# Performance work log

Measured on AMD Instinct MI355X. Metric: run time of the kernel, lower is better.

Reference implementation:

```python
import jax, jax.numpy as jnp
import numpy as np

B, T_NEW, CACHED_MAX = 8, 128, 2048
D_MODEL, N_HEADS = 1024, 16
D_HEAD = D_MODEL // N_HEADS
MAX_TOTAL = CACHED_MAX + T_NEW


def rotate_half(x):
    x1, x2 = x[..., : x.shape[-1] // 2], x[..., x.shape[-1] // 2 :]
    return jnp.concatenate([-x2, x1], axis=-1)


def setup_inputs() -> dict:
    key = jax.random.key(0)
    ks = jax.random.split(key, 16)
    w_scale = D_MODEL ** -0.5  # xavier-ish
    inp = {
        "x_new": jax.random.normal(ks[0], (B, T_NEW, D_MODEL), jnp.float32),
        "past_k": jax.random.normal(ks[1], (B, N_HEADS, CACHED_MAX, D_HEAD), jnp.float32),
        "past_v": jax.random.normal(ks[2], (B, N_HEADS, CACHED_MAX, D_HEAD), jnp.float32),
        "Wq": jax.random.normal(ks[3], (D_MODEL, D_MODEL), jnp.float32) * w_scale,
        "bq": jnp.zeros((D_MODEL,), jnp.float32),
        "Wk": jax.random.normal(ks[4], (D_MODEL, D_MODEL), jnp.float32) * w_scale,
        "bk": jnp.zeros((D_MODEL,), jnp.float32),
        "Wv": jax.random.normal(ks[5], (D_MODEL, D_MODEL), jnp.float32) * w_scale,
        "bv": jnp.zeros((D_MODEL,), jnp.float32),
        "Wo": jax.random.normal(ks[6], (D_MODEL, D_MODEL), jnp.float32) * w_scale,
        "bo": jnp.zeros((D_MODEL,), jnp.float32),
        "inv_freq": 1.0 / (10000.0 ** (jnp.arange(0, D_HEAD, 2, dtype=jnp.float32) / D_HEAD)),
        # ragged lengths; >=1 so every row attends to something
        "past_lengths": jax.random.randint(ks[7], (B,), 1, CACHED_MAX + 1),
        "new_lengths": jax.random.randint(ks[8], (B,), 1, T_NEW + 1),
    }
    return inp


def _attention_fwd(x_new, past_k, past_v, Wq, bq, Wk, bk, Wv, bv, Wo, bo, inv_freq,
                   past_lengths, new_lengths):
    steps = jnp.arange(T_NEW)
    valid_new = steps[None, :] < new_lengths[:, None]            # [B, T_new]

    def proj(W, b):  # torch Linear: x @ W.T + b -> [B, H, T_new, D_head]
        y = jnp.einsum("btm,nm->btn", x_new, W) + b
        return y.reshape(B, T_NEW, N_HEADS, D_HEAD).transpose(0, 2, 1, 3)

    q, k_new, v_new = proj(Wq, bq), proj(Wk, bk), proj(Wv, bv)

    # RoPE at absolute positions past_len + step (0 where invalid)
    positions = jnp.where(valid_new, past_lengths[:, None] + steps[None, :], 0)
    freqs = positions[..., None].astype(jnp.float32) * inv_freq  # [B, T_new, D_head/2]
    emb = jnp.concatenate([freqs, freqs], axis=-1)               # [B, T_new, D_head]
    cos = jnp.cos(emb)[:, None]                                  # [B, 1, T_new, D_head]
    sin = jnp.sin(emb)[:, None]
    q = q * cos + rotate_half(q) * sin
    k_new = k_new * cos + rotate_half(k_new) * sin

    vm = valid_new[:, None, :, None].astype(q.dtype)
    q, k_new, v_new = q * vm, k_new * vm, v_new * vm

    total_lengths = past_lengths + new_lengths
    j = jnp.arange(MAX_TOTAL)
    in_past = (j[None, :] < past_lengths[:, None])[:, None, :, None]       # [B,1,MT,1]
    in_new = ((j[None, :] >= past_lengths[:, None]) &
              (j[None, :] < total_lengths[:, None]))[:, None, :, None]
    idx_new = jnp.clip(j[None, :] - past_lengths[:, None], 0, T_NEW - 1)   # [B, MT]

    past_k_pad = jnp.pad(past_k, ((0, 0), (0, 0), (0, T_NEW), (0, 0)))
    past_v_pad = jnp.pad(past_v, ((0, 0), (0, 0), (0, T_NEW), (0, 0)))
    gather = jax.vmap(lambda xb, ib: xb[:, ib])  # [H,T_new,D], [MT] -> [H,MT,D]
    k_total = jnp.where(in_past, past_k_pad, jnp.where(in_new, gather(k_new, idx_new), 0.0))
    v_total = jnp.where(in_past, past_v_pad, jnp.where(in_new, gather(v_new, idx_new), 0.0))

    attend = j[None, :] < total_lengths[:, None]                  # [B, MT]
    scores = jnp.einsum("bhqd,bhkd->bhqk", q, k_total) * (D_HEAD ** -0.5)
    neg = jnp.asarray(jnp.finfo(scores.dtype).min, scores.dtype)
    scores = jnp.where(attend[:, None, None, :], scores, neg)
    attn = jax.nn.softmax(scores, axis=-1)
    ctx = jnp.einsum("bhqk,bhkd->bhqd", attn, v_total)            # [B,H,T_new,D]

    out = ctx.transpose(0, 2, 1, 3).reshape(B, T_NEW, D_MODEL)
    out = jnp.einsum("btm,nm->btn", out, Wo) + bo
    return out * valid_new[..., None].astype(out.dtype)


def reference(x_new, past_k, past_v, Wq, bq, Wk, bk, Wv, bv, Wo, bo, inv_freq,
              past_lengths, new_lengths):
    return _attention_fwd(x_new, past_k, past_v, Wq, bq, Wk, bk, Wv, bv, Wo, bo,
                          inv_freq, past_lengths, new_lengths)
```

## Files before the change

### kernel.cpp

```cpp
#include <hip/hip_runtime.h>

#define NB 8
#define TNEW 128
#define CMAX 2048
#define DMODEL 1024
#define NH 16
#define DH 64

typedef float f32x4 __attribute__((ext_vector_type(4)));
typedef short short8 __attribute__((ext_vector_type(8)));
typedef short short4v __attribute__((ext_vector_type(4)));

__device__ __forceinline__ short f2bf(float x) {
  unsigned u = __float_as_uint(x);
  u += 0x7FFFu + ((u >> 16) & 1u);
  return (short)(u >> 16);
}
__device__ __forceinline__ float bf2f(short s) {
  return __uint_as_float(((unsigned)(unsigned short)s) << 16);
}
__device__ __forceinline__ short8 cvt8(f32x4 a, f32x4 b) {
  short8 o;
  o[0] = f2bf(a.x); o[1] = f2bf(a.y); o[2] = f2bf(a.z); o[3] = f2bf(a.w);
  o[4] = f2bf(b.x); o[5] = f2bf(b.y); o[6] = f2bf(b.z); o[7] = f2bf(b.w);
  return o;
}

#define LGKM0_BAR()                                            \
  __builtin_amdgcn_sched_barrier(0);                           \
  asm volatile("s_waitcnt lgkmcnt(0)" ::: "memory");           \
  __builtin_amdgcn_sched_barrier(0);                           \
  __builtin_amdgcn_s_barrier()
#define TAIL_BAR()                                             \
  __builtin_amdgcn_sched_barrier(0);                           \
  __builtin_amdgcn_s_barrier()

__global__ __launch_bounds__(256) void cvt5_bf16(
    const float* __restrict__ s0, const float* __restrict__ s1,
    const float* __restrict__ s2, const float* __restrict__ s3,
    const float* __restrict__ s4, short* __restrict__ dst) {
  const int seg = blockIdx.x >> 10;
  const int i = (blockIdx.x & 1023) * 256 + threadIdx.x;
  const float* src = seg == 0 ? s0 : seg == 1 ? s1 : seg == 2 ? s2 : seg == 3 ? s3 : s4;
  f32x4 v = *(const f32x4*)(src + (size_t)i * 4);
  short4v o;
  o.x = f2bf(v.x); o.y = f2bf(v.y); o.z = f2bf(v.z); o.w = f2bf(v.w);
  *(short4v*)(dst + (size_t)seg * (1u << 20) + (size_t)i * 4) = o;
}

template<int MODE>
__global__ __launch_bounds__(256) void gemm64(
    const short* __restrict__ A, const short* __restrict__ Wbase,
    void* __restrict__ Out, const float* __restrict__ bias0,
    const float* __restrict__ bias1, const float* __restrict__ bias2,
    const int* __restrict__ new_len)
{
  constexpr int LDT = 40;
  __shared__ short As[64 * LDT];
  __shared__ short Bs[64 * LDT];
  const int n0 = blockIdx.x * 64, m0 = blockIdx.y * 64, z = blockIdx.z;
  if (MODE == 0 && (m0 & 64) && new_len[m0 >> 7] <= 64) return;
  const short* Wp = Wbase + (size_t)z * (DMODEL * DMODEL);
  const float* bias = (MODE == 0) ? (z == 0 ? bias0 : (z == 1 ? bias1 : bias2)) : bias0;
  const int tid = threadIdx.x, lane = tid & 63, w = tid >> 6;
  const int wm = (w >> 1) * 32, wn = (w & 1) * 32;
  const int lr = lane & 15, lk = lane >> 4;

  const int srow = tid >> 2, soff = (tid & 3) * 8;
  const short* Ag = A  + (size_t)(m0 + srow) * DMODEL + soff;
  const short* Bg = Wp + (size_t)(n0 + srow) * DMODEL + soff;
  short* Al = As + srow * LDT + soff;
  short* Bl = Bs + srow * LDT + soff;

  short8 va0 = *(const short8*)(Ag);
  short8 vb0 = *(const short8*)(Bg);
  short8 va1, vb1;
  f32x4 acc[2][2] = {};

#define GEMM_PHASE(CURA, CURB, NXTA, NXTB, KNEXT)                          \
  {                                                                        \
    *(short8*)Al = CURA;                                                   \
    *(short8*)Bl = CURB;                                                   \
    NXTA = *(const short8*)(Ag + (KNEXT) * 32);                            \
    NXTB = *(const short8*)(Bg + (KNEXT) * 32);                            \
    LGKM0_BAR();                                                           \
    short8 af0 = *(const short8*)(As + (wm + lr) * LDT + lk * 8);          \
    short8 af1 = *(const short8*)(As + (wm + 16 + lr) * LDT + lk * 8);     \
    short8 bg0 = *(const short8*)(Bs + (wn + lr) * LDT + lk * 8);          \
    short8 bg1 = *(const short8*)(Bs + (wn + 16 + lr) * LDT + lk * 8);     \
    acc[0][0] = __builtin_amdgcn_mfma_f32_16x16x32_bf16(af0, bg0, acc[0][0], 0, 0, 0); \
    acc[0][1] = __builtin_amdgcn_mfma_f32_16x16x32_bf16(af0, bg1, acc[0][1], 0, 0, 0); \
    acc[1][0] = __builtin_amdgcn_mfma_f32_16x16x32_bf16(af1, bg0, acc[1][0], 0, 0, 0); \
    acc[1][1] = __builtin_amdgcn_mfma_f32_16x16x32_bf16(af1, bg1, acc[1][1], 0, 0, 0); \
    TAIL_BAR();                                                            \
  }

  for (int kt = 0; kt < DMODEL / 32; kt += 2) {
    const int k1 = kt + 1;
    const int k2 = (kt + 2 < DMODEL / 32) ? kt + 2 : DMODEL / 32 - 1;
    GEMM_PHASE(va0, vb0, va1, vb1, k1);
    GEMM_PHASE(va1, vb1, va0, vb0, k2);
  }
#undef GEMM_PHASE

#pragma unroll
  for (int i = 0; i < 2; ++i) {
#pragma unroll
    for (int j = 0; j < 2; ++j) {
      const int col = n0 + wn + j * 16 + lr;
      const float bcol = bias[col];
#pragma unroll
      for (int r = 0; r < 4; ++r) {
        const int row = m0 + wm + i * 16 + lk * 4 + r;
        float v = acc[i][j][r] + bcol;
        if (MODE == 0) {
          ((short*)Out)[(size_t)z * (NB * TNEW * DMODEL) + (size_t)row * DMODEL + col] = f2bf(v);
        } else {
          const int bb = row >> 7, t = row & 127;
          ((float*)Out)[(size_t)row * DMODEL + col] = (t < new_len[bb]) ? v : 0.0f;
        }
      }
    }
  }
}

__global__ __launch_bounds__(256) void rope_mask(
    short* __restrict__ qb, short* __restrict__ kb, short* __restrict__ vb,
    const float* __restrict__ inv_freq, const int* __restrict__ past_len,
    const int* __restrict__ new_len)
{
  const int idx = blockIdx.x * 256 + threadIdx.x;
  const int d = idx & 31;
  const int h = (idx >> 5) & 15;
  const int t = (idx >> 9) & 127;
  const int b = idx >> 16;
  const bool valid = t < new_len[b];
  const float pos = (float)(past_len[b] + t);
  float sn, cs;
  sincosf(pos * inv_freq[d], &sn, &cs);
  const size_t base = (size_t)(b * 128 + t) * DMODEL + h * 64 + d;
  const float q1 = bf2f(qb[base]), q2 = bf2f(qb[base + 32]);
  const float k1 = bf2f(kb[base]), k2 = bf2f(kb[base + 32]);
  qb[base]      = valid ? f2bf(q1 * cs - q2 * sn) : (short)0;
  qb[base + 32] = valid ? f2bf(q2 * cs + q1 * sn) : (short)0;
  kb[base]      = valid ? f2bf(k1 * cs - k2 * sn) : (short)0;
  kb[base + 32] = valid ? f2bf(k2 * cs + k1 * sn) : (short)0;
  if (!valid) { vb[base] = 0; vb[base + 32] = 0; }
}

__global__ __launch_bounds__(512) void attn_split(
    const float* __restrict__ pk, const float* __restrict__ pv,
    const short* __restrict__ qb, const short* __restrict__ kb,
    const short* __restrict__ vb, float* __restrict__ Opart,
    float* __restrict__ Ml, const int* __restrict__ past_len,
    const int* __restrict__ new_len, int splits)
{
  constexpr int LDT = 72;
  __shared__ short Kl[64 * LDT];
  __shared__ short Vt[64 * LDT];
  __shared__ short Pl[128 * LDT];
  const int bh = blockIdx.x, b = bh >> 4, h = bh & 15;
  const int s = blockIdx.y;
  const int past = past_len[b];
  const int nlen = new_len[b];
  const int total = past + nlen;
  const int tid = threadIdx.x, lane = tid & 63, w = tid >> 6;
  const int lr = lane & 15, lk = lane >> 4;

  const int nt = (total + 63) >> 6;

  float* mlp = Ml + (size_t)(bh * splits + s) * 256;
  float* op  = Opart + (size_t)(bh * splits + s) * (128 * 64);

  if (s >= nt) {
#pragma unroll
    for (int r = 0; r < 4; ++r) {
      const int q = w * 16 + lk * 4 + r;
      if (lr == 0) { mlp[q] = -3.0e38f; mlp[128 + q] = 0.f; }
    }
    return;
  }

  const bool wvalid = (w * 16) < nlen;
  short8 qf0 = {}, qf1 = {};
  if (wvalid) {
    const short* qrow = qb + (size_t)(b * 128 + w * 16 + lr) * DMODEL + h * 64;
    qf0 = *(const short8*)(qrow + lk * 8);
    qf1 = *(const short8*)(qrow + 32 + lk * 8);
  }
  float m_run[4], l_run[4];
  f32x4 acc[4] = {};
#pragma unroll
  for (int r = 0; r < 4; ++r) { m_run[r] = -3.0e38f; l_run[r] = 0.f; }

  const int jr = tid >> 3, seg = tid & 7;
  const float* pkb = pk + ((size_t)(b * 16 + h) * CMAX) * 64 + seg * 8;
  const float* pvb = pv + ((size_t)(b * 16 + h) * CMAX) * 64 + seg * 8;
  const short* kbb = kb + (size_t)(b * 128) * DMODEL + h * 64 + seg * 8;
  const short* vbb = vb + (size_t)(b * 128) * DMODEL + h * 64 + seg * 8;

  f32x4 kA0 = {}, kB0 = {}, vA0 = {}, vB0 = {};
  f32x4 kA1 = {}, kB1 = {}, vA1 = {}, vB1 = {};
  int smode0 = 2, smode1 = 2;

#define STAGE_ISSUE(SET, T)                                                   \
  {                                                                           \
    const int j_ = (T) * 64 + jr;                                             \
    if (j_ < past) {                                                          \
      smode##SET = 0;                                                         \
      kA##SET = *(const f32x4*)(pkb + (size_t)j_ * 64);                       \
      kB##SET = *(const f32x4*)(pkb + (size_t)j_ * 64 + 4);                   \
      vA##SET = *(const f32x4*)(pvb + (size_t)j_ * 64);                       \
      vB##SET = *(const f32x4*)(pvb + (size_t)j_ * 64 + 4);                   \
    } else if (j_ < total) {                                                  \
      smode##SET = 1;                                                         \
      kA##SET = __builtin_bit_cast(f32x4, *(const short8*)(kbb + (size_t)(j_ - past) * DMODEL)); \
      vA##SET = __builtin_bit_cast(f32x4, *(const short8*)(vbb + (size_t)(j_ - past) * DMODEL)); \
    } else {                                                                  \
      smode##SET = 2;                                                         \
    }                                                                         \
  }

#define ATTN_TILE(SET, OTHER, KT)                                             \
  {                                                                           \
         \
    short8 kr = {}, vr = {};                                                  \
    if (smode##SET == 0) { kr = cvt8(kA##SET, kB##SET); vr = cvt8(vA##SET, vB##SET); } \
    else if (smode##SET == 1) { kr = __builtin_bit_cast(short8, kA##SET); vr = __builtin_bit_cast(short8, vA##SET); } \
    *(short8*)(Kl + jr * LDT + seg * 8) = kr;                                 \
    _Pragma("unroll")                                                         \
    for (int i = 0; i < 8; ++i) Vt[(seg * 8 + i) * LDT + (jr ^ (seg * 8))] = vr[i]; \
                    \
    STAGE_ISSUE(OTHER, (KT) + splits);                                        \
    LGKM0_BAR();                                                              \
    if (wvalid) {                                                             \
      f32x4 sc[4];                                                            \
      __builtin_amdgcn_s_setprio(1);                                          \
      _Pragma("unroll")                                                       \
      for (int nf = 0; nf < 4; ++nf) {                                        \
        short8 k0 = *(const short8*)(Kl + (nf * 16 + lr) * LDT + lk * 8);     \
        short8 k1 = *(const short8*)(Kl + (nf * 16 + lr) * LDT + 32 + lk * 8);\
        f32x4 zv = {};                                                        \
        zv = __builtin_amdgcn_mfma_f32_16x16x32_bf16(qf0, k0, zv, 0, 0, 0);   \
        sc[nf] = __builtin_amdgcn_mfma_f32_16x16x32_bf16(qf1, k1, zv, 0, 0, 0);\
      }                                                                       \
      __builtin_amdgcn_s_setprio(0);                                          \
      const int kg0 = (KT) * 64;                                              \
      float pmax[4] = {-3.0e38f, -3.0e38f, -3.0e38f, -3.0e38f};               \
      _Pragma("unroll")                                                       \
      for (int nf = 0; nf < 4; ++nf) {                                        \
        const bool ok = (kg0 + nf * 16 + lr) < total;                         \
        _Pragma("unroll")                                                     \
        for (int r = 0; r < 4; ++r) {                                         \
          const float sv = ok ? sc[nf][r] * 0.125f : -3.0e38f;                \
          sc[nf][r] = sv;                                                     \
          pmax[r] = fmaxf(pmax[r], sv);                                       \
        }                                                                     \
      }                                                                       \
      _Pragma("unroll")                                                       \
      for (int r = 0; r < 4; ++r) {                                           \
        _Pragma("unroll")                                                     \
        for (int off = 1; off < 16; off <<= 1)                                \
          pmax[r] = fmaxf(pmax[r], __shfl_xor(pmax[r], off));                 \
      }                                                                       \
      float alpha[4], rsum[4];                                                \
      _Pragma("unroll")                                                       \
      for (int r = 0; r < 4; ++r) {                                           \
        const float mn = fmaxf(m_run[r], pmax[r]);                            \
        alpha[r] = __expf(m_run[r] - mn);                                     \
        m_run[r] = mn;                                                        \
        rsum[r] = 0.f;                                                        \
      }                                                                       \
      _Pragma("unroll")                                                       \
      for (int nf = 0; nf < 4; ++nf)                                          \
        _Pragma("unroll")                                                     \
        for (int r = 0; r < 4; ++r) {                                         \
          const float p = __expf(sc[nf][r] - m_run[r]);                       \
          sc[nf][r] = p;                                                      \
          rsum[r] += p;                                                       \
        }                                                                     \
      _Pragma("unroll")                                                       \
      for (int r = 0; r < 4; ++r) {                                           \
        _Pragma("unroll")                                                     \
        for (int off = 1; off < 16; off <<= 1)                                \
          rsum[r] += __shfl_xor(rsum[r], off);                                \
        l_run[r] = l_run[r] * alpha[r] + rsum[r];                             \
      }                                                                       \
      _Pragma("unroll")                                                       \
      for (int nf = 0; nf < 4; ++nf)                                          \
        _Pragma("unroll")                                                     \
        for (int r = 0; r < 4; ++r) acc[nf][r] *= alpha[r];                   \
      _Pragma("unroll")                                                       \
      for (int nf = 0; nf < 4; ++nf)                                          \
        _Pragma("unroll")                                                     \
        for (int r = 0; r < 4; ++r)                                           \
          Pl[(w * 16 + lk * 4 + r) * LDT + nf * 16 + lr] = f2bf(sc[nf][r]);   \
      __builtin_amdgcn_s_setprio(1);                                          \
      _Pragma("unroll")                                                       \
      for (int kf = 0; kf < 2; ++kf) {                                        \
        short8 pf = *(const short8*)(Pl + (w * 16 + lr) * LDT + kf * 32 + lk * 8); \
        _Pragma("unroll")                                                     \
        for (int nf = 0; nf < 4; ++nf) {                                      \
          const int dd = nf * 16 + lr;                                        \
          short8 vf = *(const short8*)(Vt + dd * LDT + ((kf * 32 + lk * 8) ^ (dd & 56))); \
          acc[nf] = __builtin_amdgcn_mfma_f32_16x16x32_bf16(pf, vf, acc[nf], 0, 0, 0); \
        }                                                                     \
      }                                                                       \
      __builtin_amdgcn_s_setprio(0);                                          \
    }                                                                         \
    TAIL_BAR();                                                               \
  }

  STAGE_ISSUE(0, s);
  const int nIter = (nt - s + splits - 1) / splits;
  const int E = (nIter + 1) & ~1;
  for (int i = 0; i < E; i += 2) {
    const int kt0 = s + i * splits;
    ATTN_TILE(0, 1, kt0);
    ATTN_TILE(1, 0, kt0 + splits);
  }
#undef ATTN_TILE
#undef STAGE_ISSUE

  if (wvalid) {
#pragma unroll
    for (int nf = 0; nf < 4; ++nf)
#pragma unroll
      for (int r = 0; r < 4; ++r) {
        const int q = w * 16 + lk * 4 + r, d = nf * 16 + lr;
        op[(size_t)q * 64 + d] = acc[nf][r];
      }
#pragma unroll
    for (int r = 0; r < 4; ++r) {
      const int q = w * 16 + lk * 4 + r;
      if (lr == 0) { mlp[q] = m_run[r]; mlp[128 + q] = l_run[r]; }
    }
  } else {
#pragma unroll
    for (int r = 0; r < 4; ++r) {
      const int q = w * 16 + lk * 4 + r;
      if (lr == 0) { mlp[q] = -3.0e38f; mlp[128 + q] = 0.f; }
    }
  }
}

__global__ __launch_bounds__(256) void attn_combine(
    const float* __restrict__ Opart, const float* __restrict__ Ml,
    short* __restrict__ ctxb, const int* __restrict__ new_len, int splits)
{
  const int bh = blockIdx.x, b = bh >> 4, h = bh & 15;
  const int q = blockIdx.y * 16 + (threadIdx.x >> 4);
  if (q >= new_len[b]) return;
  const int dv = (threadIdx.x & 15) * 4;
  const float* mlb = Ml + (size_t)bh * splits * 256;
  float mstar = -3.0e38f;
  for (int s = 0; s < splits; ++s)
    mstar = fmaxf(mstar, mlb[s * 256 + q]);
  float lsum = 0.f;
  f32x4 o = {};
  for (int s = 0; s < splits; ++s) {
    const float ws = __expf(mlb[s * 256 + q] - mstar);
    lsum += ws * mlb[s * 256 + 128 + q];
    if (ws > 0.f) {
      f32x4 ov = *(const f32x4*)(Opart + ((size_t)(bh * splits + s) * 128 + q) * 64 + dv);
      o.x += ws * ov.x; o.y += ws * ov.y; o.z += ws * ov.z; o.w += ws * ov.w;
    }
  }
  const float inv = 1.0f / lsum;
  short4v r;
  r.x = f2bf(o.x * inv); r.y = f2bf(o.y * inv); r.z = f2bf(o.z * inv); r.w = f2bf(o.w * inv);
  *(short4v*)(ctxb + (size_t)(b * 128 + q) * DMODEL + h * 64 + dv) = r;
}

extern "C" void kernel_launch(void* const* d_in, const int* in_sizes, int n_in,
                              void* d_out, int out_size, void* d_ws, size_t ws_size,
                              hipStream_t stream) {
  const float* x      = (const float*)d_in[0];
  const float* past_k = (const float*)d_in[1];
  const float* past_v = (const float*)d_in[2];
  const float* Wq = (const float*)d_in[3];
  const float* bq = (const float*)d_in[4];
  const float* Wk = (const float*)d_in[5];
  const float* bk = (const float*)d_in[6];
  const float* Wv = (const float*)d_in[7];
  const float* bv = (const float*)d_in[8];
  const float* Wo = (const float*)d_in[9];
  const float* bo = (const float*)d_in[10];
  const float* inv_freq = (const float*)d_in[11];
  const int* past_len = (const int*)d_in[12];
  const int* new_len  = (const int*)d_in[13];

  short* wsb = (short*)d_ws;
  const size_t M1 = 1u << 20;
  short* Xb  = wsb;
  short* Wqb = wsb + 1 * M1;
  short* Wob = wsb + 4 * M1;
  short* qb  = wsb + 5 * M1;
  short* kb  = wsb + 6 * M1;
  short* vb  = wsb + 7 * M1;
  short* ctx = wsb + 8 * M1;
  float* Opart = (float*)(wsb + 9 * M1);

  int splits = 1;
  for (int s = 8; s >= 1; s >>= 1) {
    size_t need = 9 * M1 * sizeof(short) +
                  (size_t)s * 128 * (128 * 64 + 256) * sizeof(float);
    if (need <= ws_size) { splits = s; break; }
  }
  float* Ml = Opart + (size_t)128 * splits * (128 * 64);

  cvt5_bf16<<<5120, 256, 0, stream>>>(x, Wq, Wk, Wv, Wo, wsb);

  gemm64<0><<<dim3(16, 16, 3), 256, 0, stream>>>(Xb, Wqb, (void*)qb, bq, bk, bv, new_len);
  rope_mask<<<2048, 256, 0, stream>>>(qb, kb, vb, inv_freq, past_len, new_len);
  attn_split<<<dim3(128, splits), 512, 0, stream>>>(past_k, past_v, qb, kb, vb,
                                                    Opart, Ml, past_len, new_len, splits);
  attn_combine<<<dim3(128, 8), 256, 0, stream>>>(Opart, Ml, ctx, new_len, splits);
  gemm64<1><<<dim3(16, 16, 1), 256, 0, stream>>>(ctx, Wob, d_out, bo, nullptr, nullptr, new_len);
}
```

Baseline: 79.63 us.

## Fuse RoPE into QKV projection epilogue and flatten attention split grid

Removes the separate rope_mask kernel. The Q/K GEMM epilogue now applies the rotary embedding directly, using a changed warp column mapping so each lane holds both d and d+32 of a head. This removes one launch and a read-modify-write pass over the bf16 Q/K/V buffers. The attention launch is flattened to a 1D grid with splits interleaved per (batch, head), and a guard skips compute on tiles past the valid length. Invalid new-token rows of q/k/v are no longer explicitly zeroed, so the code now relies on downstream masking to keep them out of the result.

```diff
diff --git a/kernel.cpp b/kernel.cpp
--- a/kernel.cpp
+++ b/kernel.cpp
@@ -53,7 +53,8 @@
     const short* __restrict__ A, const short* __restrict__ Wbase,
     void* __restrict__ Out, const float* __restrict__ bias0,
     const float* __restrict__ bias1, const float* __restrict__ bias2,
-    const int* __restrict__ new_len)
+    const int* __restrict__ new_len, const float* __restrict__ inv_freq,
+    const int* __restrict__ past_len)
 {
   constexpr int LDT = 40;
   __shared__ short As[64 * LDT];
@@ -63,7 +64,7 @@
   const short* Wp = Wbase + (size_t)z * (DMODEL * DMODEL);
   const float* bias = (MODE == 0) ? (z == 0 ? bias0 : (z == 1 ? bias1 : bias2)) : bias0;
   const int tid = threadIdx.x, lane = tid & 63, w = tid >> 6;
-  const int wm = (w >> 1) * 32, wn = (w & 1) * 32;
+  const int wm = (w >> 1) * 32, wn2 = (w & 1) * 16;
   const int lr = lane & 15, lk = lane >> 4;
 
   const int srow = tid >> 2, soff = (tid & 3) * 8;
@@ -86,8 +87,8 @@
     LGKM0_BAR();                                                           \
     short8 af0 = *(const short8*)(As + (wm + lr) * LDT + lk * 8);          \
     short8 af1 = *(const short8*)(As + (wm + 16 + lr) * LDT + lk * 8);     \
-    short8 bg0 = *(const short8*)(Bs + (wn + lr) * LDT + lk * 8);          \
-    short8 bg1 = *(const short8*)(Bs + (wn + 16 + lr) * LDT + lk * 8);     \
+    short8 bg0 = *(const short8*)(Bs + (wn2 + lr) * LDT + lk * 8);         \
+    short8 bg1 = *(const short8*)(Bs + (wn2 + 32 + lr) * LDT + lk * 8);    \
     acc[0][0] = __builtin_amdgcn_mfma_f32_16x16x32_bf16(af0, bg0, acc[0][0], 0, 0, 0); \
     acc[0][1] = __builtin_amdgcn_mfma_f32_16x16x32_bf16(af0, bg1, acc[0][1], 0, 0, 0); \
     acc[1][0] = __builtin_amdgcn_mfma_f32_16x16x32_bf16(af1, bg0, acc[1][0], 0, 0, 0); \
@@ -103,49 +104,49 @@
   }
 #undef GEMM_PHASE
 
-#pragma unroll
-  for (int i = 0; i < 2; ++i) {
-#pragma unroll
-    for (int j = 0; j < 2; ++j) {
-      const int col = n0 + wn + j * 16 + lr;
-      const float bcol = bias[col];
+  const int colb = n0 + wn2 + lr;
+  const float b0 = bias[colb], b1 = bias[colb + 32];
+
+  if (MODE == 0 && z <= 1) {
+    const int bb = m0 >> 7;
+    const int pbase = past_len[bb];
+    const float fr = inv_freq[(wn2 + lr) & 31];
+    short* outp = (short*)Out + (size_t)z * (NB * TNEW * DMODEL);
+#pragma unroll
+    for (int i = 0; i < 2; ++i) {
 #pragma unroll
       for (int r = 0; r < 4; ++r) {
         const int row = m0 + wm + i * 16 + lk * 4 + r;
-        float v = acc[i][j][r] + bcol;
+        const float pos = (float)(pbase + (row & 127));
+        float sn, cs;
+        sincosf(pos * fr, &sn, &cs);
+        const float a0 = acc[i][0][r] + b0;
+        const float a1 = acc[i][1][r] + b1;
+        outp[(size_t)row * DMODEL + colb]      = f2bf(a0 * cs - a1 * sn);
+        outp[(size_t)row * DMODEL + colb + 32] = f2bf(a1 * cs + a0 * sn);
+      }
+    }
+  } else {
+#pragma unroll
+    for (int i = 0; i < 2; ++i) {
+#pragma unroll
+      for (int r = 0; r < 4; ++r) {
+        const int row = m0 + wm + i * 16 + lk * 4 + r;
+        const float a0 = acc[i][0][r] + b0;
+        const float a1 = acc[i][1][r] + b1;
         if (MODE == 0) {
-          ((short*)Out)[(size_t)z * (NB * TNEW * DMODEL) + (size_t)row * DMODEL + col] = f2bf(v);
+          short* outp = (short*)Out + (size_t)z * (NB * TNEW * DMODEL);
+          outp[(size_t)row * DMODEL + colb]      = f2bf(a0);
+          outp[(size_t)row * DMODEL + colb + 32] = f2bf(a1);
         } else {
           const int bb = row >> 7, t = row & 127;
-          ((float*)Out)[(size_t)row * DMODEL + col] = (t < new_len[bb]) ? v : 0.0f;
+          const bool ok = t < new_len[bb];
+          ((float*)Out)[(size_t)row * DMODEL + colb]      = ok ? a0 : 0.0f;
+          ((float*)Out)[(size_t)row * DMODEL + colb + 32] = ok ? a1 : 0.0f;
         }
       }
     }
   }
-}
-
-__global__ __launch_bounds__(256) void rope_mask(
-    short* __restrict__ qb, short* __restrict__ kb, short* __restrict__ vb,
-    const float* __restrict__ inv_freq, const int* __restrict__ past_len,
-    const int* __restrict__ new_len)
-{
-  const int idx = blockIdx.x * 256 + threadIdx.x;
-  const int d = idx & 31;
-  const int h = (idx >> 5) & 15;
-  const int t = (idx >> 9) & 127;
-  const int b = idx >> 16;
-  const bool valid = t < new_len[b];
-  const float pos = (float)(past_len[b] + t);
-  float sn, cs;
-  sincosf(pos * inv_freq[d], &sn, &cs);
-  const size_t base = (size_t)(b * 128 + t) * DMODEL + h * 64 + d;
-  const float q1 = bf2f(qb[base]), q2 = bf2f(qb[base + 32]);
-  const float k1 = bf2f(kb[base]), k2 = bf2f(kb[base + 32]);
-  qb[base]      = valid ? f2bf(q1 * cs - q2 * sn) : (short)0;
-  qb[base + 32] = valid ? f2bf(q2 * cs + q1 * sn) : (short)0;
-  kb[base]      = valid ? f2bf(k1 * cs - k2 * sn) : (short)0;
-  kb[base + 32] = valid ? f2bf(k2 * cs + k1 * sn) : (short)0;
-  if (!valid) { vb[base] = 0; vb[base + 32] = 0; }
 }
 
 __global__ __launch_bounds__(512) void attn_split(
@@ -159,8 +160,9 @@
   __shared__ short Kl[64 * LDT];
   __shared__ short Vt[64 * LDT];
   __shared__ short Pl[128 * LDT];
-  const int bh = blockIdx.x, b = bh >> 4, h = bh & 15;
-  const int s = blockIdx.y;
+  const int id = blockIdx.x;
+  const int bh = id / splits, s = id - bh * splits;
+  const int b = bh >> 4, h = bh & 15;
   const int past = past_len[b];
   const int nlen = new_len[b];
   const int total = past + nlen;
@@ -221,7 +223,7 @@
     }                                                                         \
   }
 
-#define ATTN_TILE(SET, OTHER, KT)                                             \
+#define ATTN_TILE(SET, OTHER, KT)                                            \
   {                                                                           \
          \
     short8 kr = {}, vr = {};                                                  \
@@ -233,7 +235,7 @@
                     \
     STAGE_ISSUE(OTHER, (KT) + splits);                                        \
     LGKM0_BAR();                                                              \
-    if (wvalid) {                                                             \
+    if (wvalid && (KT) < nt) {                                                \
       f32x4 sc[4];                                                            \
       __builtin_amdgcn_s_setprio(1);                                          \
       _Pragma("unroll")                                                       \
@@ -411,10 +413,11 @@
 
   cvt5_bf16<<<5120, 256, 0, stream>>>(x, Wq, Wk, Wv, Wo, wsb);
 
-  gemm64<0><<<dim3(16, 16, 3), 256, 0, stream>>>(Xb, Wqb, (void*)qb, bq, bk, bv, new_len);
-  rope_mask<<<2048, 256, 0, stream>>>(qb, kb, vb, inv_freq, past_len, new_len);
-  attn_split<<<dim3(128, splits), 512, 0, stream>>>(past_k, past_v, qb, kb, vb,
-                                                    Opart, Ml, past_len, new_len, splits);
+  gemm64<0><<<dim3(16, 16, 3), 256, 0, stream>>>(Xb, Wqb, (void*)qb, bq, bk, bv,
+                                                 new_len, inv_freq, past_len);
+  attn_split<<<128 * splits, 512, 0, stream>>>(past_k, past_v, qb, kb, vb,
+                                               Opart, Ml, past_len, new_len, splits);
   attn_combine<<<dim3(128, 8), 256, 0, stream>>>(Opart, Ml, ctx, new_len, splits);
-  gemm64<1><<<dim3(16, 16, 1), 256, 0, stream>>>(ctx, Wob, d_out, bo, nullptr, nullptr, new_len);
-}
+  gemm64<1><<<dim3(16, 16, 1), 256, 0, stream>>>(ctx, Wob, d_out, bo, nullptr, nullptr,
+                                                 new_len, nullptr, nullptr);
+}
```

Result: faster. 75.61 us (-5.1%).
